# Kernel tuning notes

Hardware: AMD Instinct MI355X
Metric: run time of the kernel (lower is better)

Reference implementation:

```python
import jax, jax.numpy as jnp
import numpy as np

V = 50257   # vocab_size
BLOCK = 1024
D = 768     # n_embd
H = 12      # n_head
L = 2       # n_layer
B = 4
T = 1024
EPS = 1e-5


def _ln(x, g, b):
    mu = jnp.mean(x, axis=-1, keepdims=True)
    var = jnp.var(x, axis=-1, keepdims=True)
    return (x - mu) * jax.lax.rsqrt(var + EPS) * g + b


def setup_inputs() -> dict:
    key = jax.random.key(0)
    ks = jax.random.split(key, 10)
    def n(k, shape, std=0.02):
        return jax.random.normal(k, shape, jnp.float32) * std
    proj_std = (2 * L) ** -0.5  # set_scale init in the torch code
    return dict(
        idx=jax.random.randint(ks[0], (B, T), 0, V),
        layer_num=0,
        wte=n(ks[1], (V, D)),
        wpe=n(ks[2], (BLOCK, D)),
        ln1_g=jnp.ones((L, D)), ln1_b=jnp.zeros((L, D)),
        attn_w=n(ks[3], (L, D, 3 * D)), attn_b=jnp.zeros((L, 3 * D)),
        proj_w=n(ks[4], (L, D, D), proj_std), proj_b=jnp.zeros((L, D)),
        ln2_g=jnp.ones((L, D)), ln2_b=jnp.zeros((L, D)),
        fc_w=n(ks[5], (L, D, 4 * D)), fc_b=jnp.zeros((L, 4 * D)),
        fc2_w=n(ks[6], (L, 4 * D, D), proj_std), fc2_b=jnp.zeros((L, D)),
        lnf_g=jnp.ones((D,)), lnf_b=jnp.zeros((D,)),
        lm_w=n(ks[7], (D, V)),
    )


def _gpt(idx, wte, wpe, ln1_g, ln1_b, attn_w, attn_b, proj_w, proj_b,
         ln2_g, ln2_b, fc_w, fc_b, fc2_w, fc2_b, lnf_g, lnf_b, lm_w):
    b, t = idx.shape
    hd = D // H
    x = wte[idx] + wpe[:t]                      # [B,T,D]
    causal = jnp.tril(jnp.ones((t, t), bool))   # [T,T]
    for l in range(L):
        h = _ln(x, ln1_g[l], ln1_b[l])
        qkv = h @ attn_w[l] + attn_b[l]          # [B,T,3D]
        q, k, v = jnp.split(qkv, 3, axis=-1)
        q = q.reshape(b, t, H, hd)
        k = k.reshape(b, t, H, hd)
        v = v.reshape(b, t, H, hd)
        att = jnp.einsum('bqhd,bkhd->bhqk', q, k) * (1.0 / np.sqrt(hd))
        att = jnp.where(causal, att, -jnp.inf)
        att = jax.nn.softmax(att, axis=-1)
        y = jnp.einsum('bhqk,bkhd->bqhd', att, v).reshape(b, t, D)
        x = x + (y @ proj_w[l] + proj_b[l])
        h2 = _ln(x, ln2_g[l], ln2_b[l])
        h2 = jax.nn.gelu(h2 @ fc_w[l] + fc_b[l], approximate=True)  # tanh GELU
        x = x + (h2 @ fc2_w[l] + fc2_b[l])
    x = _ln(x, lnf_g, lnf_b)
    return x @ lm_w                             # [B,T,V] logits


def reference(idx, layer_num, wte, wpe, ln1_g, ln1_b, attn_w, attn_b,
              proj_w, proj_b, ln2_g, ln2_b, fc_w, fc_b, fc2_w, fc2_b,
              lnf_g, lnf_b, lm_w):
    # layer_num is unused in the forward math (pipeline-stage bookkeeping)
    return _gpt(idx, wte, wpe, ln1_g, ln1_b, attn_w, attn_b, proj_w, proj_b,
                ln2_g, ln2_b, fc_w, fc_b, fc2_w, fc2_b, lnf_g, lnf_b, lm_w)
```

## Files before the change

### kernel.cpp

```cpp
#include <hip/hip_runtime.h>
#include <hip/hip_bf16.h>
#include <cstdint>
#include <cstddef>

typedef __bf16 bf16_t;
typedef __bf16 bf16x8 __attribute__((ext_vector_type(8)));
typedef float f32x4 __attribute__((ext_vector_type(4)));

#define GLB_AS(p) ((__attribute__((address_space(1))) void*)(void*)(p))
#define LDS_AS(p) ((__attribute__((address_space(3))) void*)(p))

__device__ __forceinline__ float wave_red_sum(float v) {
#pragma unroll
  for (int o = 1; o < 64; o <<= 1) v += __shfl_xor(v, o, 64);
  return v;
}

__device__ __forceinline__ float gelu_tanh(float v) {
  float c = 0.7978845608028654f * (v + 0.044715f * v * v * v);
  return 0.5f * v * (1.0f + tanhf(c));
}

__global__ __launch_bounds__(256) void embed_k(const int* __restrict__ idx,
                                               const float* __restrict__ wte,
                                               const float* __restrict__ wpe,
                                               float* __restrict__ x) {
  const int m = blockIdx.x;
  const int tid = threadIdx.x;
  const int tok = idx[m];
  const int t = m & 1023;
#pragma unroll
  for (int i = 0; i < 3; ++i) {
    const int d = tid + i * 256;
    x[(size_t)m * 768 + d] = wte[(size_t)tok * 768 + d] + wpe[(size_t)t * 768 + d];
  }
}

__global__ __launch_bounds__(256) void ln_k(const float* __restrict__ x,
                                            const float* __restrict__ g,
                                            const float* __restrict__ b,
                                            bf16_t* __restrict__ out) {
  const int row = blockIdx.x;
  const int tid = threadIdx.x;
  const float* xr = x + (size_t)row * 768;
  float v0 = xr[tid], v1 = xr[tid + 256], v2 = xr[tid + 512];
  float s = v0 + v1 + v2;
  float q = v0 * v0 + v1 * v1 + v2 * v2;
  s = wave_red_sum(s);
  q = wave_red_sum(q);
  __shared__ float sm[8];
  const int wave = tid >> 6, lane = tid & 63;
  if (lane == 0) { sm[wave] = s; sm[4 + wave] = q; }
  __syncthreads();
  s = sm[0] + sm[1] + sm[2] + sm[3];
  q = sm[4] + sm[5] + sm[6] + sm[7];
  const float mu = s * (1.0f / 768.0f);
  const float var = q * (1.0f / 768.0f) - mu * mu;
  const float rs = rsqrtf(var + 1e-5f);
  bf16_t* orow = out + (size_t)row * 768;
#pragma unroll
  for (int i = 0; i < 3; ++i) {
    const int d = tid + i * 256;
    const float v = (i == 0 ? v0 : (i == 1 ? v1 : v2));
    orow[d] = (bf16_t)((v - mu) * rs * g[d] + b[d]);
  }
}

__global__ __launch_bounds__(256) void transp_k(const float* __restrict__ W,
                                                bf16_t* __restrict__ WT,
                                                int K, int N, int Npad) {
  __shared__ float tile[32][33];
  const int n0 = blockIdx.x * 32, k0 = blockIdx.y * 32;
  const int tx = threadIdx.x, ty = threadIdx.y;
#pragma unroll
  for (int i = 0; i < 4; ++i) {
    const int k = k0 + ty + i * 8, n = n0 + tx;
    tile[ty + i * 8][tx] = (k < K && n < N) ? W[(size_t)k * N + n] : 0.0f;
  }
  __syncthreads();
#pragma unroll
  for (int i = 0; i < 4; ++i) {
    const int n = n0 + ty + i * 8, k = k0 + tx;
    if (n < Npad && k < K) WT[(size_t)n * K + k] = (bf16_t)tile[tx][ty + i * 8];
  }
}

__global__ __launch_bounds__(256) void vtr_k(const bf16_t* __restrict__ qkv,
                                             bf16_t* __restrict__ vt) {
  __shared__ bf16_t tile[64][72];
  const int bh = blockIdx.y;
  const int h = bh % 12, b = bh / 12;
  const int t0 = blockIdx.x * 64;
  const int tx = threadIdx.x & 63;
  const int wv = threadIdx.x >> 6;
#pragma unroll
  for (int i = 0; i < 16; ++i) {
    const int r = wv * 16 + i;
    tile[r][tx] = qkv[(size_t)(b * 1024 + t0 + r) * 2304 + 1536 + h * 64 + tx];
  }
  __syncthreads();
#pragma unroll
  for (int i = 0; i < 16; ++i) {
    const int d = wv * 16 + i;
    vt[((size_t)bh * 64 + d) * 1024 + t0 + tx] = tile[tx][d];
  }
}

template <int EPI>
__global__ __launch_bounds__(256) void gemm_bt(const bf16_t* __restrict__ A,
                                               const bf16_t* __restrict__ BT,
                                               const float* __restrict__ bias,
                                               void* __restrict__ outp,
                                               float* __restrict__ resid,
                                               int M, int N, int K, int Nout) {
  __shared__ __align__(16) bf16_t As[128 * 32];
  __shared__ __align__(16) bf16_t Bs[128 * 32];
  const int tid = threadIdx.x;
  const int lane = tid & 63, wave = tid >> 6;

  const int nmblk = M >> 7;
  const int nwg = gridDim.x;
  const int flat = blockIdx.x;
  const int xcd = flat & 7, rest = flat >> 3;
  const int q8 = nwg >> 3, r8 = nwg & 7;
  const int wgid = (xcd < r8 ? xcd * (q8 + 1) : r8 * (q8 + 1) + (xcd - r8) * q8) + rest;
  const int m0 = (wgid % nmblk) * 128;
  const int n0 = (wgid / nmblk) * 128;

  const int wr = wave >> 1, wc = wave & 1;
  const int fr = lane & 15, fq = lane >> 4;
  const int se = tid * 8;
  const int srow = se >> 5, scol = se & 31;
  const int wvbase = wave * 512;
  f32x4 acc[4][4] = {};

  for (int k0 = 0; k0 < K; k0 += 32) {
#pragma unroll
    for (int r = 0; r < 2; ++r) {
      __builtin_amdgcn_global_load_lds(
          GLB_AS(&A[(size_t)(m0 + srow + r * 64) * K + k0 + scol]),
          LDS_AS(&As[wvbase + r * 2048]), 16, 0, 0);
      __builtin_amdgcn_global_load_lds(
          GLB_AS(&BT[(size_t)(n0 + srow + r * 64) * K + k0 + scol]),
          LDS_AS(&Bs[wvbase + r * 2048]), 16, 0, 0);
    }
    __syncthreads();
    bf16x8 a[4], b[4];
#pragma unroll
    for (int i = 0; i < 4; ++i) {
      a[i] = *(const bf16x8*)(&As[(wr * 64 + i * 16 + fr) * 32 + fq * 8]);
      b[i] = *(const bf16x8*)(&Bs[(wc * 64 + i * 16 + fr) * 32 + fq * 8]);
    }
#pragma unroll
    for (int i = 0; i < 4; ++i)
#pragma unroll
      for (int j = 0; j < 4; ++j)
        acc[i][j] = __builtin_amdgcn_mfma_f32_16x16x32_bf16(a[i], b[j], acc[i][j], 0, 0, 0);
    __syncthreads();
  }

#pragma unroll
  for (int i = 0; i < 4; ++i) {
#pragma unroll
    for (int j = 0; j < 4; ++j) {
      const int r0 = m0 + wr * 64 + i * 16 + fq * 4;
      const int c = n0 + wc * 64 + j * 16 + fr;
      float bv = 0.0f;
      if constexpr (EPI != 3) bv = bias[c];
#pragma unroll
      for (int e = 0; e < 4; ++e) {
        const int r = r0 + e;
        float v = acc[i][j][e] + bv;
        if constexpr (EPI == 0) {
          ((bf16_t*)outp)[(size_t)r * N + c] = (bf16_t)v;
        } else if constexpr (EPI == 1) {
          ((bf16_t*)outp)[(size_t)r * N + c] = (bf16_t)gelu_tanh(v);
        } else if constexpr (EPI == 2) {
          resid[(size_t)r * N + c] += v;
        } else {
          if (c < Nout) ((float*)outp)[(size_t)r * Nout + c] = v;
        }
      }
    }
  }
}

__global__ __launch_bounds__(256) void fattn_k(const bf16_t* __restrict__ qkv,
                                               const bf16_t* __restrict__ vt,
                                               bf16_t* __restrict__ y) {
  __shared__ bf16_t Pl[4][16][40];
  const int wave = threadIdx.x >> 6, lane = threadIdx.x & 63;
  const int wid = blockIdx.x * 4 + wave;
  const int qt = wid & 63;
  const int bh = wid >> 6;
  const int h = bh % 12, b = bh / 12;
  const int fr = lane & 15, fq = lane >> 4;

  const bf16_t* qrow = qkv + (size_t)(b * 1024 + qt * 16 + fr) * 2304 + h * 64;
  const bf16x8 qf0 = *(const bf16x8*)(qrow + fq * 8);
  const bf16x8 qf1 = *(const bf16x8*)(qrow + 32 + fq * 8);

  const bf16_t* kbase = qkv + (size_t)b * 1024 * 2304 + 768 + h * 64 + fq * 8;
  const bf16_t* vbase = vt + ((size_t)bh * 64 + fr) * 1024 + fq * 8;

  f32x4 o[4] = {};
  float mrun[4], lrun[4];
#pragma unroll
  for (int e = 0; e < 4; ++e) { mrun[e] = -1e30f; lrun[e] = 0.0f; }

  const int qg = qt * 16 + fq * 4;
  const int kv_end = qt * 16 + 16;

  for (int kv0 = 0; kv0 < kv_end; kv0 += 32) {
    f32x4 s0 = {}, s1 = {};
    {
      const bf16_t* k0p = kbase + (size_t)(kv0 + fr) * 2304;
      const bf16_t* k1p = kbase + (size_t)(kv0 + 16 + fr) * 2304;
      const bf16x8 kf00 = *(const bf16x8*)(k0p);
      const bf16x8 kf01 = *(const bf16x8*)(k0p + 32);
      const bf16x8 kf10 = *(const bf16x8*)(k1p);
      const bf16x8 kf11 = *(const bf16x8*)(k1p + 32);
      s0 = __builtin_amdgcn_mfma_f32_16x16x32_bf16(qf0, kf00, s0, 0, 0, 0);
      s0 = __builtin_amdgcn_mfma_f32_16x16x32_bf16(qf1, kf01, s0, 0, 0, 0);
      s1 = __builtin_amdgcn_mfma_f32_16x16x32_bf16(qf0, kf10, s1, 0, 0, 0);
      s1 = __builtin_amdgcn_mfma_f32_16x16x32_bf16(qf1, kf11, s1, 0, 0, 0);
    }
    float v0[4], v1[4];
#pragma unroll
    for (int e = 0; e < 4; ++e) {
      v0[e] = (kv0 + fr <= qg + e) ? s0[e] * 0.125f : -1e30f;
      v1[e] = (kv0 + 16 + fr <= qg + e) ? s1[e] * 0.125f : -1e30f;
    }
    float p0[4], p1[4];
#pragma unroll
    for (int e = 0; e < 4; ++e) {
      float mx = fmaxf(v0[e], v1[e]);
      mx = fmaxf(mx, __shfl_xor(mx, 1, 64));
      mx = fmaxf(mx, __shfl_xor(mx, 2, 64));
      mx = fmaxf(mx, __shfl_xor(mx, 4, 64));
      mx = fmaxf(mx, __shfl_xor(mx, 8, 64));
      const float mnew = fmaxf(mrun[e], mx);
      p0[e] = __expf(v0[e] - mnew);
      p1[e] = __expf(v1[e] - mnew);
      float rs = p0[e] + p1[e];
      rs += __shfl_xor(rs, 1, 64);
      rs += __shfl_xor(rs, 2, 64);
      rs += __shfl_xor(rs, 4, 64);
      rs += __shfl_xor(rs, 8, 64);
      const float alpha = __expf(mrun[e] - mnew);
      lrun[e] = lrun[e] * alpha + rs;
      mrun[e] = mnew;
#pragma unroll
      for (int db = 0; db < 4; ++db) o[db][e] *= alpha;
    }
#pragma unroll
    for (int e = 0; e < 4; ++e) {
      Pl[wave][fq * 4 + e][fr] = (bf16_t)p0[e];
      Pl[wave][fq * 4 + e][16 + fr] = (bf16_t)p1[e];
    }
    asm volatile("s_waitcnt lgkmcnt(0)" ::: "memory");
    const bf16x8 pf = *(const bf16x8*)(&Pl[wave][fr][fq * 8]);
#pragma unroll
    for (int db = 0; db < 4; ++db) {
      const bf16x8 vf = *(const bf16x8*)(vbase + (size_t)db * 16 * 1024 + kv0);
      o[db] = __builtin_amdgcn_mfma_f32_16x16x32_bf16(pf, vf, o[db], 0, 0, 0);
    }
  }

#pragma unroll
  for (int db = 0; db < 4; ++db) {
#pragma unroll
    for (int e = 0; e < 4; ++e) {
      const int q = qt * 16 + fq * 4 + e;
      const int d = db * 16 + fr;
      y[(size_t)(b * 1024 + q) * 768 + h * 64 + d] = (bf16_t)(o[db][e] / lrun[e]);
    }
  }
}

extern "C" void kernel_launch(void* const* d_in, const int* in_sizes, int n_in,
                              void* d_out, int out_size, void* d_ws, size_t ws_size,
                              hipStream_t stream) {
  constexpr int Bb = 4, T = 1024, Lg = 2, Vr = 50257, Vp = 50304;
  constexpr int M = Bb * T;

  const int* idx = (const int*)d_in[0];
  const float* wte = (const float*)d_in[2];
  const float* wpe = (const float*)d_in[3];
  const float* ln1_g = (const float*)d_in[4];
  const float* ln1_b = (const float*)d_in[5];
  const float* attn_w = (const float*)d_in[6];
  const float* attn_b = (const float*)d_in[7];
  const float* proj_w = (const float*)d_in[8];
  const float* proj_b = (const float*)d_in[9];
  const float* ln2_g = (const float*)d_in[10];
  const float* ln2_b = (const float*)d_in[11];
  const float* fc_w = (const float*)d_in[12];
  const float* fc_b = (const float*)d_in[13];
  const float* fc2_w = (const float*)d_in[14];
  const float* fc2_b = (const float*)d_in[15];
  const float* lnf_g = (const float*)d_in[16];
  const float* lnf_b = (const float*)d_in[17];
  const float* lm_w = (const float*)d_in[18];
  float* out = (float*)d_out;

  char* wp = (char*)d_ws;
  auto take = [&](size_t n) { char* p = wp; wp += (n + 255) & ~(size_t)255; return p; };
  bf16_t* WqkvT = (bf16_t*)take((size_t)Lg * 2304 * 768 * 2);
  bf16_t* WprojT = (bf16_t*)take((size_t)Lg * 768 * 768 * 2);
  bf16_t* WfcT = (bf16_t*)take((size_t)Lg * 3072 * 768 * 2);
  bf16_t* Wfc2T = (bf16_t*)take((size_t)Lg * 768 * 3072 * 2);
  bf16_t* WlmT = (bf16_t*)take((size_t)Vp * 768 * 2);
  float* xb = (float*)take((size_t)M * 768 * 4);
  bf16_t* hb = (bf16_t*)take((size_t)M * 768 * 2);
  bf16_t* qkvb = (bf16_t*)take((size_t)M * 2304 * 2);
  bf16_t* yb = (bf16_t*)take((size_t)M * 768 * 2);
  bf16_t* actb = (bf16_t*)take((size_t)M * 3072 * 2);
  bf16_t* vtb = (bf16_t*)take((size_t)M * 768 * 2);

  const dim3 tb(32, 8);
  for (int l = 0; l < Lg; ++l) {
    transp_k<<<dim3(2304 / 32, 768 / 32), tb, 0, stream>>>(
        attn_w + (size_t)l * 768 * 2304, WqkvT + (size_t)l * 2304 * 768, 768, 2304, 2304);
    transp_k<<<dim3(768 / 32, 768 / 32), tb, 0, stream>>>(
        proj_w + (size_t)l * 768 * 768, WprojT + (size_t)l * 768 * 768, 768, 768, 768);
    transp_k<<<dim3(3072 / 32, 768 / 32), tb, 0, stream>>>(
        fc_w + (size_t)l * 768 * 3072, WfcT + (size_t)l * 3072 * 768, 768, 3072, 3072);
    transp_k<<<dim3(768 / 32, 3072 / 32), tb, 0, stream>>>(
        fc2_w + (size_t)l * 3072 * 768, Wfc2T + (size_t)l * 768 * 3072, 3072, 768, 768);
  }
  transp_k<<<dim3(Vp / 32, 768 / 32), tb, 0, stream>>>(lm_w, WlmT, 768, Vr, Vp);

  embed_k<<<M, 256, 0, stream>>>(idx, wte, wpe, xb);

  for (int l = 0; l < Lg; ++l) {
    ln_k<<<M, 256, 0, stream>>>(xb, ln1_g + l * 768, ln1_b + l * 768, hb);
    gemm_bt<0><<<(M / 128) * (2304 / 128), 256, 0, stream>>>(
        hb, WqkvT + (size_t)l * 2304 * 768, attn_b + l * 2304, qkvb, nullptr,
        M, 2304, 768, 2304);
    vtr_k<<<dim3(T / 64, Bb * 12), 256, 0, stream>>>(qkvb, vtb);
    fattn_k<<<(Bb * 12 * 64) / 4, 256, 0, stream>>>(qkvb, vtb, yb);
    gemm_bt<2><<<(M / 128) * (768 / 128), 256, 0, stream>>>(
        yb, WprojT + (size_t)l * 768 * 768, proj_b + l * 768, nullptr, xb,
        M, 768, 768, 768);
    ln_k<<<M, 256, 0, stream>>>(xb, ln2_g + l * 768, ln2_b + l * 768, hb);
    gemm_bt<1><<<(M / 128) * (3072 / 128), 256, 0, stream>>>(
        hb, WfcT + (size_t)l * 3072 * 768, fc_b + l * 3072, actb, nullptr,
        M, 3072, 768, 3072);
    gemm_bt<2><<<(M / 128) * (768 / 128), 256, 0, stream>>>(
        actb, Wfc2T + (size_t)l * 768 * 3072, fc2_b + l * 768, nullptr, xb,
        M, 768, 3072, 768);
  }
  ln_k<<<M, 256, 0, stream>>>(xb, lnf_g, lnf_b, hb);
  gemm_bt<3><<<(M / 128) * (Vp / 128), 256, 0, stream>>>(
      hb, WlmT, nullptr, out, nullptr, M, Vp, 768, Vr);
}
```

Baseline: 1.355 ms.

## Add 256x256-tile pipelined GEMM for QKV, FC and LM-head projections

Introduces a new 512-thread GEMM kernel with 256x256 output tiles, BK=64, double-buffered LDS staging via direct global-to-LDS loads, an XOR swizzle to avoid bank conflicts, and interleaved barriers with s_setprio around MFMA phases. The QKV, FC and LM-head GEMMs use it, while the residual-add GEMMs keep the old 128x128 kernel, which is now specialised to the residual epilogue. The vocab padding grows to a multiple of 256 to match the new tile. Larger tiles raise data reuse and overlap loads with compute, at the cost of 128KB LDS per block and fewer blocks for the smaller GEMMs.

```diff
diff --git a/kernel.cpp b/kernel.cpp
--- a/kernel.cpp
+++ b/kernel.cpp
@@ -9,6 +9,7 @@
 
 #define GLB_AS(p) ((__attribute__((address_space(1))) void*)(void*)(p))
 #define LDS_AS(p) ((__attribute__((address_space(3))) void*)(p))
+#define PIN(x) asm volatile("" : "+v"(x))
 
 __device__ __forceinline__ float wave_red_sum(float v) {
 #pragma unroll
@@ -19,6 +20,11 @@
 __device__ __forceinline__ float gelu_tanh(float v) {
   float c = 0.7978845608028654f * (v + 0.044715f * v * v * v);
   return 0.5f * v * (1.0f + tanhf(c));
+}
+
+__device__ __forceinline__ f32x4 mfma16(f32x4 a, f32x4 b, f32x4 c) {
+  return __builtin_amdgcn_mfma_f32_16x16x32_bf16(
+      __builtin_bit_cast(bf16x8, a), __builtin_bit_cast(bf16x8, b), c, 0, 0, 0);
 }
 
 __global__ __launch_bounds__(256) void embed_k(const int* __restrict__ idx,
@@ -107,6 +113,165 @@
 }
 
 template <int EPI>
+__global__ __launch_bounds__(512, 2) void gemm256(const bf16_t* __restrict__ A,
+                                                  const bf16_t* __restrict__ BT,
+                                                  const float* __restrict__ bias,
+                                                  void* __restrict__ outp,
+                                                  int M, int N, int K, int Nout) {
+  __shared__ __align__(16) char lds[131072];
+  const int tid = threadIdx.x;
+  const int lane = tid & 63, wave = tid >> 6;
+  const int wr = wave >> 2, wc = wave & 3;
+  const int fr = lane & 15, fq = lane >> 4;
+
+  const int nmblk = M >> 8;
+  const int nwg = gridDim.x;
+  const int flat = blockIdx.x;
+  const int xcd = flat & 7, rest = flat >> 3;
+  const int q8 = nwg >> 3, r8 = nwg & 7;
+  const int wgid = (xcd < r8 ? xcd * (q8 + 1) : r8 * (q8 + 1) + (xcd - r8) * q8) + rest;
+  const int m0 = (wgid % nmblk) << 8;
+  const int n0 = (wgid / nmblk) << 8;
+
+  const int NT = K >> 6;
+
+  int srow[4], scb[4];
+#pragma unroll
+  for (int u = 0; u < 4; ++u) {
+    const int Lb = u * 8192 + tid * 16;
+    const int s = Lb ^ (((Lb >> 9) & 1) << 5);
+    srow[u] = s >> 7;
+    scb[u] = s & 127;
+  }
+  const char* Abase = (const char*)A;
+  const char* Bbase = (const char*)BT;
+
+  auto stageA = [&](int pi, int u, int tau) {
+    const char* src = Abase + ((size_t)(m0 + srow[u]) * K + tau * 64) * 2 + scb[u];
+    __builtin_amdgcn_global_load_lds(GLB_AS(src),
+        LDS_AS(&lds[pi * 32768 + u * 8192 + wave * 1024]), 16, 0, 0);
+  };
+  auto stageB = [&](int pi, int u, int tau) {
+    const char* src = Bbase + ((size_t)(n0 + srow[u]) * K + tau * 64) * 2 + scb[u];
+    __builtin_amdgcn_global_load_lds(GLB_AS(src),
+        LDS_AS(&lds[65536 + pi * 32768 + u * 8192 + wave * 1024]), 16, 0, 0);
+  };
+  auto rdA = [&](int pi, int msub, int i, int kk) -> f32x4 {
+    const int row = wr * 128 + msub * 64 + i * 16 + fr;
+    const int off = (row * 128 + kk * 64 + fq * 16) ^ (((row >> 2) & 1) << 5);
+    return *(const f32x4*)(&lds[pi * 32768 + off]);
+  };
+  auto rdB = [&](int pi, int j, int kk) -> f32x4 {
+    const int row = wc * 64 + j * 16 + fr;
+    const int off = (row * 128 + kk * 64 + fq * 16) ^ (((row >> 2) & 1) << 5);
+    return *(const f32x4*)(&lds[65536 + pi * 32768 + off]);
+  };
+
+  f32x4 acc[8][4] = {};
+  f32x4 a_[4][2], b_[4][2];
+
+  stageA(0, 0, 0); stageA(0, 1, 0); stageA(0, 2, 0); stageA(0, 3, 0);
+  stageB(0, 0, 0); stageB(0, 1, 0); stageB(0, 2, 0); stageB(0, 3, 0);
+  stageA(1, 0, 1); stageA(1, 2, 1); stageB(1, 0, 1); stageB(1, 1, 1);
+  stageA(1, 1, 1); stageA(1, 3, 1);
+  asm volatile("s_waitcnt vmcnt(6)" ::: "memory");
+  __builtin_amdgcn_s_barrier();
+
+  int pi = 0;
+  for (int tau = 0; tau < NT; ++tau) {
+#pragma unroll
+    for (int i = 0; i < 4; ++i) { a_[i][0] = rdA(pi, 0, i, 0); a_[i][1] = rdA(pi, 0, i, 1); }
+#pragma unroll
+    for (int j = 0; j < 4; ++j) { b_[j][0] = rdB(pi, j, 0); b_[j][1] = rdB(pi, j, 1); }
+#pragma unroll
+    for (int i = 0; i < 4; ++i) { PIN(a_[i][0]); PIN(a_[i][1]); }
+#pragma unroll
+    for (int j = 0; j < 4; ++j) { PIN(b_[j][0]); PIN(b_[j][1]); }
+    if (tau + 1 < NT) { stageB(pi ^ 1, 2, tau + 1); stageB(pi ^ 1, 3, tau + 1); }
+    __builtin_amdgcn_s_barrier();
+    __builtin_amdgcn_s_setprio(1);
+#pragma unroll
+    for (int i = 0; i < 4; ++i)
+#pragma unroll
+      for (int j = 0; j < 2; ++j) {
+        acc[i][j] = mfma16(a_[i][0], b_[j][0], acc[i][j]);
+        acc[i][j] = mfma16(a_[i][1], b_[j][1], acc[i][j]);
+      }
+    __builtin_amdgcn_s_setprio(0);
+    __builtin_amdgcn_s_barrier();
+    if (tau + 2 < NT) { stageA(pi, 0, tau + 2); stageA(pi, 2, tau + 2); }
+    __builtin_amdgcn_s_barrier();
+    __builtin_amdgcn_s_setprio(1);
+#pragma unroll
+    for (int i = 0; i < 4; ++i)
+#pragma unroll
+      for (int j = 0; j < 2; ++j) {
+        acc[i][2 + j] = mfma16(a_[i][0], b_[2 + j][0], acc[i][2 + j]);
+        acc[i][2 + j] = mfma16(a_[i][1], b_[2 + j][1], acc[i][2 + j]);
+      }
+    __builtin_amdgcn_s_setprio(0);
+    __builtin_amdgcn_s_barrier();
+#pragma unroll
+    for (int i = 0; i < 4; ++i) { a_[i][0] = rdA(pi, 1, i, 0); a_[i][1] = rdA(pi, 1, i, 1); }
+#pragma unroll
+    for (int i = 0; i < 4; ++i) { PIN(a_[i][0]); PIN(a_[i][1]); }
+    if (tau + 2 < NT) { stageB(pi, 0, tau + 2); stageB(pi, 1, tau + 2); }
+    __builtin_amdgcn_s_barrier();
+    __builtin_amdgcn_s_setprio(1);
+#pragma unroll
+    for (int i = 0; i < 4; ++i)
+#pragma unroll
+      for (int j = 0; j < 2; ++j) {
+        acc[4 + i][j] = mfma16(a_[i][0], b_[j][0], acc[4 + i][j]);
+        acc[4 + i][j] = mfma16(a_[i][1], b_[j][1], acc[4 + i][j]);
+      }
+    __builtin_amdgcn_s_setprio(0);
+    __builtin_amdgcn_s_barrier();
+    if (tau + 2 < NT) {
+      stageA(pi, 1, tau + 2); stageA(pi, 3, tau + 2);
+      asm volatile("s_waitcnt vmcnt(6)" ::: "memory");
+    } else {
+      asm volatile("s_waitcnt vmcnt(0)" ::: "memory");
+    }
+    __builtin_amdgcn_s_barrier();
+    __builtin_amdgcn_s_setprio(1);
+#pragma unroll
+    for (int i = 0; i < 4; ++i)
+#pragma unroll
+      for (int j = 0; j < 2; ++j) {
+        acc[4 + i][2 + j] = mfma16(a_[i][0], b_[2 + j][0], acc[4 + i][2 + j]);
+        acc[4 + i][2 + j] = mfma16(a_[i][1], b_[2 + j][1], acc[4 + i][2 + j]);
+      }
+    __builtin_amdgcn_s_setprio(0);
+    __builtin_amdgcn_s_barrier();
+    pi ^= 1;
+  }
+
+#pragma unroll
+  for (int i8 = 0; i8 < 8; ++i8) {
+#pragma unroll
+    for (int j4 = 0; j4 < 4; ++j4) {
+      const int r0 = m0 + wr * 128 + i8 * 16 + fq * 4;
+      const int c = n0 + wc * 64 + j4 * 16 + fr;
+      float bv = 0.0f;
+      if constexpr (EPI != 3) bv = bias[c];
+#pragma unroll
+      for (int e = 0; e < 4; ++e) {
+        const int r = r0 + e;
+        float v = acc[i8][j4][e] + bv;
+        if constexpr (EPI == 0) {
+          ((bf16_t*)outp)[(size_t)r * N + c] = (bf16_t)v;
+        } else if constexpr (EPI == 1) {
+          ((bf16_t*)outp)[(size_t)r * N + c] = (bf16_t)gelu_tanh(v);
+        } else {
+          if (c < Nout) ((float*)outp)[(size_t)r * Nout + c] = v;
+        }
+      }
+    }
+  }
+}
+
+template <int EPI>
 __global__ __launch_bounds__(256) void gemm_bt(const bf16_t* __restrict__ A,
                                                const bf16_t* __restrict__ BT,
                                                const float* __restrict__ bias,
@@ -165,21 +330,11 @@
     for (int j = 0; j < 4; ++j) {
       const int r0 = m0 + wr * 64 + i * 16 + fq * 4;
       const int c = n0 + wc * 64 + j * 16 + fr;
-      float bv = 0.0f;
-      if constexpr (EPI != 3) bv = bias[c];
+      const float bv = bias[c];
 #pragma unroll
       for (int e = 0; e < 4; ++e) {
         const int r = r0 + e;
-        float v = acc[i][j][e] + bv;
-        if constexpr (EPI == 0) {
-          ((bf16_t*)outp)[(size_t)r * N + c] = (bf16_t)v;
-        } else if constexpr (EPI == 1) {
-          ((bf16_t*)outp)[(size_t)r * N + c] = (bf16_t)gelu_tanh(v);
-        } else if constexpr (EPI == 2) {
-          resid[(size_t)r * N + c] += v;
-        } else {
-          if (c < Nout) ((float*)outp)[(size_t)r * Nout + c] = v;
-        }
+        resid[(size_t)r * N + c] += acc[i][j][e] + bv;
       }
     }
   }
@@ -281,7 +436,7 @@
 extern "C" void kernel_launch(void* const* d_in, const int* in_sizes, int n_in,
                               void* d_out, int out_size, void* d_ws, size_t ws_size,
                               hipStream_t stream) {
-  constexpr int Bb = 4, T = 1024, Lg = 2, Vr = 50257, Vp = 50304;
+  constexpr int Bb = 4, T = 1024, Lg = 2, Vr = 50257, Vp = 50432;
   constexpr int M = Bb * T;
 
   const int* idx = (const int*)d_in[0];
@@ -335,23 +490,21 @@
 
   for (int l = 0; l < Lg; ++l) {
     ln_k<<<M, 256, 0, stream>>>(xb, ln1_g + l * 768, ln1_b + l * 768, hb);
-    gemm_bt<0><<<(M / 128) * (2304 / 128), 256, 0, stream>>>(
-        hb, WqkvT + (size_t)l * 2304 * 768, attn_b + l * 2304, qkvb, nullptr,
-        M, 2304, 768, 2304);
+    gemm256<0><<<(M / 256) * (2304 / 256), 512, 0, stream>>>(
+        hb, WqkvT + (size_t)l * 2304 * 768, attn_b + l * 2304, qkvb, M, 2304, 768, 2304);
     vtr_k<<<dim3(T / 64, Bb * 12), 256, 0, stream>>>(qkvb, vtb);
     fattn_k<<<(Bb * 12 * 64) / 4, 256, 0, stream>>>(qkvb, vtb, yb);
     gemm_bt<2><<<(M / 128) * (768 / 128), 256, 0, stream>>>(
         yb, WprojT + (size_t)l * 768 * 768, proj_b + l * 768, nullptr, xb,
         M, 768, 768, 768);
     ln_k<<<M, 256, 0, stream>>>(xb, ln2_g + l * 768, ln2_b + l * 768, hb);
-    gemm_bt<1><<<(M / 128) * (3072 / 128), 256, 0, stream>>>(
-        hb, WfcT + (size_t)l * 3072 * 768, fc_b + l * 3072, actb, nullptr,
-        M, 3072, 768, 3072);
+    gemm256<1><<<(M / 256) * (3072 / 256), 512, 0, stream>>>(
+        hb, WfcT + (size_t)l * 3072 * 768, fc_b + l * 3072, actb, M, 3072, 768, 3072);
     gemm_bt<2><<<(M / 128) * (768 / 128), 256, 0, stream>>>(
         actb, Wfc2T + (size_t)l * 768 * 3072, fc2_b + l * 768, nullptr, xb,
         M, 768, 3072, 768);
   }
   ln_k<<<M, 256, 0, stream>>>(xb, lnf_g, lnf_b, hb);
-  gemm_bt<3><<<(M / 128) * (Vp / 128), 256, 0, stream>>>(
-      hb, WlmT, nullptr, out, nullptr, M, Vp, 768, Vr);
-}
+  gemm256<3><<<(M / 256) * (Vp / 256), 512, 0, stream>>>(
+      hb, WlmT, nullptr, out, M, Vp, 768, Vr);
+}
```

After: 1.301 ms. 4.0% less time.

## Replace GEMM with 256x128 double-buffered swizzled-LDS kernel using 8 waves

Applied to the files above, without the earlier changes.

Swaps the 128x128 single-buffered GEMM for a 256x128 tile kernel with 512 threads. It double-buffers LDS with global_load_lds prefetch two K-steps ahead, XOR-swizzles the LDS layout to avoid bank conflicts, and splits the MFMA work into two halves with barriers and setprio. The aim is to overlap global loads with MFMA compute and raise the compute-to-load ratio. Vocab padding grows to a multiple of 128 per the new tiling, and logits use nontemporal stores. Hand-placed waitcnt and barrier scheduling risks correctness and pipeline hazards.

```diff
diff --git a/kernel.cpp b/kernel.cpp
--- a/kernel.cpp
+++ b/kernel.cpp
@@ -9,6 +9,7 @@
 
 #define GLB_AS(p) ((__attribute__((address_space(1))) void*)(void*)(p))
 #define LDS_AS(p) ((__attribute__((address_space(3))) void*)(p))
+#define PIN(x) asm volatile("" : "+v"(x))
 
 __device__ __forceinline__ float wave_red_sum(float v) {
 #pragma unroll
@@ -20,6 +21,13 @@
   float c = 0.7978845608028654f * (v + 0.044715f * v * v * v);
   return 0.5f * v * (1.0f + tanhf(c));
 }
+
+__device__ __forceinline__ f32x4 mfma16(f32x4 a, f32x4 b, f32x4 c) {
+  return __builtin_amdgcn_mfma_f32_16x16x32_bf16(
+      __builtin_bit_cast(bf16x8, a), __builtin_bit_cast(bf16x8, b), c, 0, 0, 0);
+}
+
+__device__ __forceinline__ int swz(int off) { return off ^ ((off >> 3) & 0x30); }
 
 __global__ __launch_bounds__(256) void embed_k(const int* __restrict__ idx,
                                                const float* __restrict__ wte,
@@ -107,66 +115,122 @@
 }
 
 template <int EPI>
-__global__ __launch_bounds__(256) void gemm_bt(const bf16_t* __restrict__ A,
-                                               const bf16_t* __restrict__ BT,
-                                               const float* __restrict__ bias,
-                                               void* __restrict__ outp,
-                                               float* __restrict__ resid,
-                                               int M, int N, int K, int Nout) {
-  __shared__ __align__(16) bf16_t As[128 * 32];
-  __shared__ __align__(16) bf16_t Bs[128 * 32];
+__global__ __launch_bounds__(512, 4) void gemm256(const bf16_t* __restrict__ A,
+                                                  const bf16_t* __restrict__ BT,
+                                                  const float* __restrict__ bias,
+                                                  void* __restrict__ outp,
+                                                  float* __restrict__ resid,
+                                                  int M, int N, int K, int Nout) {
+  __shared__ __align__(16) char lds[49152];
   const int tid = threadIdx.x;
   const int lane = tid & 63, wave = tid >> 6;
-
-  const int nmblk = M >> 7;
+  const int wr = wave >> 2, wc = wave & 3;
+  const int fr = lane & 15, fq = lane >> 4;
+
+  const int nmblk = M >> 8;
   const int nwg = gridDim.x;
   const int flat = blockIdx.x;
   const int xcd = flat & 7, rest = flat >> 3;
   const int q8 = nwg >> 3, r8 = nwg & 7;
   const int wgid = (xcd < r8 ? xcd * (q8 + 1) : r8 * (q8 + 1) + (xcd - r8) * q8) + rest;
-  const int m0 = (wgid % nmblk) * 128;
-  const int n0 = (wgid / nmblk) * 128;
-
-  const int wr = wave >> 1, wc = wave & 1;
-  const int fr = lane & 15, fq = lane >> 4;
-  const int se = tid * 8;
-  const int srow = se >> 5, scol = se & 31;
-  const int wvbase = wave * 512;
-  f32x4 acc[4][4] = {};
-
-  for (int k0 = 0; k0 < K; k0 += 32) {
-#pragma unroll
-    for (int r = 0; r < 2; ++r) {
-      __builtin_amdgcn_global_load_lds(
-          GLB_AS(&A[(size_t)(m0 + srow + r * 64) * K + k0 + scol]),
-          LDS_AS(&As[wvbase + r * 2048]), 16, 0, 0);
-      __builtin_amdgcn_global_load_lds(
-          GLB_AS(&BT[(size_t)(n0 + srow + r * 64) * K + k0 + scol]),
-          LDS_AS(&Bs[wvbase + r * 2048]), 16, 0, 0);
-    }
-    __syncthreads();
-    bf16x8 a[4], b[4];
+  const int m0 = (wgid % nmblk) << 8;
+  const int n0 = (wgid / nmblk) << 7;
+
+  const int NT = K >> 5;
+
+  int srowA[2], scbA[2], srowB, scbB;
+#pragma unroll
+  for (int u = 0; u < 2; ++u) {
+    const int s = swz(u * 8192 + tid * 16);
+    srowA[u] = s >> 6;
+    scbA[u] = s & 63;
+  }
+  {
+    const int s = swz(tid * 16);
+    srowB = s >> 6;
+    scbB = s & 63;
+  }
+  const char* Abase = (const char*)A;
+  const char* Bbase = (const char*)BT;
+
+  int offA[8], offB[2];
+#pragma unroll
+  for (int i = 0; i < 8; ++i) {
+    const int row = wr * 128 + i * 16 + fr;
+    offA[i] = swz(row * 64 + fq * 16);
+  }
+#pragma unroll
+  for (int j = 0; j < 2; ++j) {
+    const int row = wc * 32 + j * 16 + fr;
+    offB[j] = 32768 + swz(row * 64 + fq * 16);
+  }
+
+  auto stageA = [&](int pi, int u, int tau) {
+    const char* src = Abase + ((size_t)(m0 + srowA[u]) * K + tau * 32) * 2 + scbA[u];
+    __builtin_amdgcn_global_load_lds(GLB_AS(src),
+        LDS_AS(&lds[pi * 16384 + u * 8192 + wave * 1024]), 16, 0, 0);
+  };
+  auto stageB = [&](int pi, int tau) {
+    const char* src = Bbase + ((size_t)(n0 + srowB) * K + tau * 32) * 2 + scbB;
+    __builtin_amdgcn_global_load_lds(GLB_AS(src),
+        LDS_AS(&lds[32768 + pi * 8192 + wave * 1024]), 16, 0, 0);
+  };
+
+  f32x4 acc[8][2] = {};
+
+  stageA(0, 0, 0); stageA(0, 1, 0); stageB(0, 0);
+  stageA(1, 0, 1); stageA(1, 1, 1); stageB(1, 1);
+  asm volatile("s_waitcnt vmcnt(3)" ::: "memory");
+  __builtin_amdgcn_s_barrier();
+
+  int pi = 0;
+  for (int tau = 0; tau < NT; ++tau) {
+    const int aoff = pi * 16384, boff = pi * 8192;
+    f32x4 aM[8], bb[2];
+#pragma unroll
+    for (int i = 0; i < 8; ++i) aM[i] = *(const f32x4*)(&lds[offA[i] + aoff]);
+#pragma unroll
+    for (int j = 0; j < 2; ++j) bb[j] = *(const f32x4*)(&lds[offB[j] + boff]);
+#pragma unroll
+    for (int i = 0; i < 8; ++i) PIN(aM[i]);
+    PIN(bb[0]); PIN(bb[1]);
+    __builtin_amdgcn_s_barrier();
+    asm volatile("s_waitcnt lgkmcnt(0)" ::: "memory");
+    __builtin_amdgcn_sched_barrier(0);
+    __builtin_amdgcn_s_setprio(1);
 #pragma unroll
     for (int i = 0; i < 4; ++i) {
-      a[i] = *(const bf16x8*)(&As[(wr * 64 + i * 16 + fr) * 32 + fq * 8]);
-      b[i] = *(const bf16x8*)(&Bs[(wc * 64 + i * 16 + fr) * 32 + fq * 8]);
-    }
-#pragma unroll
-    for (int i = 0; i < 4; ++i)
-#pragma unroll
-      for (int j = 0; j < 4; ++j)
-        acc[i][j] = __builtin_amdgcn_mfma_f32_16x16x32_bf16(a[i], b[j], acc[i][j], 0, 0, 0);
-    __syncthreads();
-  }
-
-#pragma unroll
-  for (int i = 0; i < 4; ++i) {
-#pragma unroll
-    for (int j = 0; j < 4; ++j) {
-      const int r0 = m0 + wr * 64 + i * 16 + fq * 4;
-      const int c = n0 + wc * 64 + j * 16 + fr;
+      acc[i][0] = mfma16(aM[i], bb[0], acc[i][0]);
+      acc[i][1] = mfma16(aM[i], bb[1], acc[i][1]);
+    }
+    __builtin_amdgcn_s_setprio(0);
+    __builtin_amdgcn_s_barrier();
+    if (tau + 2 < NT) {
+      stageA(pi, 0, tau + 2); stageA(pi, 1, tau + 2); stageB(pi, tau + 2);
+      asm volatile("s_waitcnt vmcnt(3)" ::: "memory");
+    } else {
+      asm volatile("s_waitcnt vmcnt(0)" ::: "memory");
+    }
+    __builtin_amdgcn_s_barrier();
+    __builtin_amdgcn_s_setprio(1);
+#pragma unroll
+    for (int i = 0; i < 4; ++i) {
+      acc[4 + i][0] = mfma16(aM[4 + i], bb[0], acc[4 + i][0]);
+      acc[4 + i][1] = mfma16(aM[4 + i], bb[1], acc[4 + i][1]);
+    }
+    __builtin_amdgcn_s_setprio(0);
+    __builtin_amdgcn_s_barrier();
+    pi ^= 1;
+  }
+
+#pragma unroll
+  for (int i = 0; i < 8; ++i) {
+#pragma unroll
+    for (int j = 0; j < 2; ++j) {
+      const int r0 = m0 + wr * 128 + i * 16 + fq * 4;
+      const int c = n0 + wc * 32 + j * 16 + fr;
       float bv = 0.0f;
-      if constexpr (EPI != 3) bv = bias[c];
+      if constexpr (EPI == 0 || EPI == 1 || EPI == 2) bv = bias[c];
 #pragma unroll
       for (int e = 0; e < 4; ++e) {
         const int r = r0 + e;
@@ -178,7 +242,8 @@
         } else if constexpr (EPI == 2) {
           resid[(size_t)r * N + c] += v;
         } else {
-          if (c < Nout) ((float*)outp)[(size_t)r * Nout + c] = v;
+          if (c < Nout)
+            __builtin_nontemporal_store(v, &((float*)outp)[(size_t)r * Nout + c]);
         }
       }
     }
@@ -281,7 +346,7 @@
 extern "C" void kernel_launch(void* const* d_in, const int* in_sizes, int n_in,
                               void* d_out, int out_size, void* d_ws, size_t ws_size,
                               hipStream_t stream) {
-  constexpr int Bb = 4, T = 1024, Lg = 2, Vr = 50257, Vp = 50304;
+  constexpr int Bb = 4, T = 1024, Lg = 2, Vr = 50257, Vp = 50432;
   constexpr int M = Bb * T;
 
   const int* idx = (const int*)d_in[0];
@@ -335,23 +400,23 @@
 
   for (int l = 0; l < Lg; ++l) {
     ln_k<<<M, 256, 0, stream>>>(xb, ln1_g + l * 768, ln1_b + l * 768, hb);
-    gemm_bt<0><<<(M / 128) * (2304 / 128), 256, 0, stream>>>(
+    gemm256<0><<<(M / 256) * (2304 / 128), 512, 0, stream>>>(
         hb, WqkvT + (size_t)l * 2304 * 768, attn_b + l * 2304, qkvb, nullptr,
         M, 2304, 768, 2304);
     vtr_k<<<dim3(T / 64, Bb * 12), 256, 0, stream>>>(qkvb, vtb);
     fattn_k<<<(Bb * 12 * 64) / 4, 256, 0, stream>>>(qkvb, vtb, yb);
-    gemm_bt<2><<<(M / 128) * (768 / 128), 256, 0, stream>>>(
+    gemm256<2><<<(M / 256) * (768 / 128), 512, 0, stream>>>(
         yb, WprojT + (size_t)l * 768 * 768, proj_b + l * 768, nullptr, xb,
         M, 768, 768, 768);
     ln_k<<<M, 256, 0, stream>>>(xb, ln2_g + l * 768, ln2_b + l * 768, hb);
-    gemm_bt<1><<<(M / 128) * (3072 / 128), 256, 0, stream>>>(
+    gemm256<1><<<(M / 256) * (3072 / 128), 512, 0, stream>>>(
         hb, WfcT + (size_t)l * 3072 * 768, fc_b + l * 3072, actb, nullptr,
         M, 3072, 768, 3072);
-    gemm_bt<2><<<(M / 128) * (768 / 128), 256, 0, stream>>>(
+    gemm256<2><<<(M / 256) * (768 / 128), 512, 0, stream>>>(
         actb, Wfc2T + (size_t)l * 768 * 3072, fc2_b + l * 768, nullptr, xb,
         M, 768, 3072, 768);
   }
   ln_k<<<M, 256, 0, stream>>>(xb, lnf_g, lnf_b, hb);
-  gemm_bt<3><<<(M / 128) * (Vp / 128), 256, 0, stream>>>(
+  gemm256<3><<<(M / 256) * (Vp / 128), 512, 0, stream>>>(
       hb, WlmT, nullptr, out, nullptr, M, Vp, 768, Vr);
 }
```

Result: slower. 1.540 ms (+13.7%).

## Add 128x256 double-buffered GEMM with direct-to-LDS loads for wide projections

Applied to the files above, without the earlier changes.

Adds a new 512-thread GEMM kernel with 128x256 tiles. It stages A and B straight into swizzled LDS through global_load_lds, double-buffers the K loop, and splits the MFMA work around the prefetch using s_setprio and explicit waitcnt. The QKV, FC and LM-head GEMMs move to this kernel, and the vocab padding grows to a multiple of 256. The aim is to hide global-load latency, avoid LDS bank conflicts and reuse more data per tile on the large GEMMs. In exchange the kernel uses more LDS and registers, and the LM head does some extra padded work.

```diff
diff --git a/kernel.cpp b/kernel.cpp
--- a/kernel.cpp
+++ b/kernel.cpp
@@ -9,6 +9,7 @@
 
 #define GLB_AS(p) ((__attribute__((address_space(1))) void*)(void*)(p))
 #define LDS_AS(p) ((__attribute__((address_space(3))) void*)(p))
+#define PIN(x) asm volatile("" : "+v"(x))
 
 __device__ __forceinline__ float wave_red_sum(float v) {
 #pragma unroll
@@ -20,6 +21,13 @@
   float c = 0.7978845608028654f * (v + 0.044715f * v * v * v);
   return 0.5f * v * (1.0f + tanhf(c));
 }
+
+__device__ __forceinline__ f32x4 mfma16(f32x4 a, f32x4 b, f32x4 c) {
+  return __builtin_amdgcn_mfma_f32_16x16x32_bf16(
+      __builtin_bit_cast(bf16x8, a), __builtin_bit_cast(bf16x8, b), c, 0, 0, 0);
+}
+
+__device__ __forceinline__ int swz(int off) { return off ^ ((off >> 3) & 0x30); }
 
 __global__ __launch_bounds__(256) void embed_k(const int* __restrict__ idx,
                                                const float* __restrict__ wte,
@@ -107,6 +115,125 @@
 }
 
 template <int EPI>
+__global__ __launch_bounds__(512, 4) void gemm256(const bf16_t* __restrict__ A,
+                                                  const bf16_t* __restrict__ BT,
+                                                  const float* __restrict__ bias,
+                                                  void* __restrict__ outp,
+                                                  int M, int N, int K, int Nout) {
+  __shared__ __align__(16) char lds[49152];
+  const int tid = threadIdx.x;
+  const int lane = tid & 63, wave = tid >> 6;
+  const int wr = wave >> 2, wc = wave & 3;
+  const int fr = lane & 15, fq = lane >> 4;
+
+  const int nmblk = M >> 7;
+  const int nwg = gridDim.x;
+  const int flat = blockIdx.x;
+  const int xcd = flat & 7, rest = flat >> 3;
+  const int q8 = nwg >> 3, r8 = nwg & 7;
+  const int wgid = (xcd < r8 ? xcd * (q8 + 1) : r8 * (q8 + 1) + (xcd - r8) * q8) + rest;
+  const int m0 = (wgid % nmblk) << 7;
+  const int n0 = (wgid / nmblk) << 8;
+
+  const int NT = K >> 5;
+
+  int srow[2], scb[2];
+#pragma unroll
+  for (int u = 0; u < 2; ++u) {
+    const int s = swz(u * 8192 + tid * 16);
+    srow[u] = s >> 6;
+    scb[u] = s & 63;
+  }
+  const char* Abase = (const char*)A;
+  const char* Bbase = (const char*)BT;
+
+  auto stageA = [&](int pi, int tau) {
+    const char* src = Abase + ((size_t)(m0 + srow[0]) * K + tau * 32) * 2 + scb[0];
+    __builtin_amdgcn_global_load_lds(GLB_AS(src),
+        LDS_AS(&lds[pi * 8192 + wave * 1024]), 16, 0, 0);
+  };
+  auto stageB = [&](int pi, int u, int tau) {
+    const char* src = Bbase + ((size_t)(n0 + srow[u]) * K + tau * 32) * 2 + scb[u];
+    __builtin_amdgcn_global_load_lds(GLB_AS(src),
+        LDS_AS(&lds[16384 + pi * 16384 + u * 8192 + wave * 1024]), 16, 0, 0);
+  };
+  auto rdA = [&](int pi, int i) -> f32x4 {
+    const int off = swz((wr * 64 + i * 16 + fr) * 64 + fq * 16);
+    return *(const f32x4*)(&lds[pi * 8192 + off]);
+  };
+  auto rdB = [&](int pi, int j) -> f32x4 {
+    const int off = swz((wc * 64 + j * 16 + fr) * 64 + fq * 16);
+    return *(const f32x4*)(&lds[16384 + pi * 16384 + off]);
+  };
+
+  f32x4 acc[4][4] = {};
+
+  stageA(0, 0); stageB(0, 0, 0); stageB(0, 1, 0);
+  stageA(1, 1); stageB(1, 0, 1); stageB(1, 1, 1);
+  asm volatile("s_waitcnt vmcnt(3)" ::: "memory");
+  __builtin_amdgcn_s_barrier();
+
+  int pi = 0;
+  for (int tau = 0; tau < NT; ++tau) {
+    f32x4 a_[4], b_[4];
+#pragma unroll
+    for (int i = 0; i < 4; ++i) a_[i] = rdA(pi, i);
+#pragma unroll
+    for (int j = 0; j < 4; ++j) b_[j] = rdB(pi, j);
+#pragma unroll
+    for (int i = 0; i < 4; ++i) { PIN(a_[i]); PIN(b_[i]); }
+    __builtin_amdgcn_s_setprio(1);
+#pragma unroll
+    for (int i = 0; i < 4; ++i) {
+      acc[i][0] = mfma16(a_[i], b_[0], acc[i][0]);
+      acc[i][1] = mfma16(a_[i], b_[1], acc[i][1]);
+    }
+    __builtin_amdgcn_s_setprio(0);
+    __builtin_amdgcn_s_barrier();
+    if (tau + 2 < NT) {
+      stageA(pi, tau + 2); stageB(pi, 0, tau + 2); stageB(pi, 1, tau + 2);
+    }
+    __builtin_amdgcn_s_setprio(1);
+#pragma unroll
+    for (int i = 0; i < 4; ++i) {
+      acc[i][2] = mfma16(a_[i], b_[2], acc[i][2]);
+      acc[i][3] = mfma16(a_[i], b_[3], acc[i][3]);
+    }
+    __builtin_amdgcn_s_setprio(0);
+    if (tau + 2 < NT) {
+      asm volatile("s_waitcnt vmcnt(3)" ::: "memory");
+    } else {
+      asm volatile("s_waitcnt vmcnt(0)" ::: "memory");
+    }
+    __builtin_amdgcn_s_barrier();
+    pi ^= 1;
+  }
+
+#pragma unroll
+  for (int i = 0; i < 4; ++i) {
+#pragma unroll
+    for (int j = 0; j < 4; ++j) {
+      const int r0 = m0 + wr * 64 + i * 16 + fq * 4;
+      const int c = n0 + wc * 64 + j * 16 + fr;
+      float bv = 0.0f;
+      if constexpr (EPI != 3) bv = bias[c];
+#pragma unroll
+      for (int e = 0; e < 4; ++e) {
+        const int r = r0 + e;
+        float v = acc[i][j][e] + bv;
+        if constexpr (EPI == 0) {
+          ((bf16_t*)outp)[(size_t)r * N + c] = (bf16_t)v;
+        } else if constexpr (EPI == 1) {
+          ((bf16_t*)outp)[(size_t)r * N + c] = (bf16_t)gelu_tanh(v);
+        } else {
+          if (c < Nout) ((float*)outp)[(size_t)r * Nout + c] = v;
+        }
+      }
+    }
+  }
+}
+
+template <int EPI>
 __global__ __launch_bounds__(256) void gemm_bt(const bf16_t* __restrict__ A,
                                                const bf16_t* __restrict__ BT,
                                                const float* __restrict__ bias,
@@ -165,21 +292,11 @@
     for (int j = 0; j < 4; ++j) {
       const int r0 = m0 + wr * 64 + i * 16 + fq * 4;
       const int c = n0 + wc * 64 + j * 16 + fr;
-      float bv = 0.0f;
-      if constexpr (EPI != 3) bv = bias[c];
+      const float bv = bias[c];
 #pragma unroll
       for (int e = 0; e < 4; ++e) {
         const int r = r0 + e;
-        float v = acc[i][j][e] + bv;
-        if constexpr (EPI == 0) {
-          ((bf16_t*)outp)[(size_t)r * N + c] = (bf16_t)v;
-        } else if constexpr (EPI == 1) {
-          ((bf16_t*)outp)[(size_t)r * N + c] = (bf16_t)gelu_tanh(v);
-        } else if constexpr (EPI == 2) {
-          resid[(size_t)r * N + c] += v;
-        } else {
-          if (c < Nout) ((float*)outp)[(size_t)r * Nout + c] = v;
-        }
+        resid[(size_t)r * N + c] += acc[i][j][e] + bv;
       }
     }
   }
@@ -281,7 +398,7 @@
 extern "C" void kernel_launch(void* const* d_in, const int* in_sizes, int n_in,
                               void* d_out, int out_size, void* d_ws, size_t ws_size,
                               hipStream_t stream) {
-  constexpr int Bb = 4, T = 1024, Lg = 2, Vr = 50257, Vp = 50304;
+  constexpr int Bb = 4, T = 1024, Lg = 2, Vr = 50257, Vp = 50432;
   constexpr int M = Bb * T;
 
   const int* idx = (const int*)d_in[0];
@@ -335,23 +452,21 @@
 
   for (int l = 0; l < Lg; ++l) {
     ln_k<<<M, 256, 0, stream>>>(xb, ln1_g + l * 768, ln1_b + l * 768, hb);
-    gemm_bt<0><<<(M / 128) * (2304 / 128), 256, 0, stream>>>(
-        hb, WqkvT + (size_t)l * 2304 * 768, attn_b + l * 2304, qkvb, nullptr,
-        M, 2304, 768, 2304);
+    gemm256<0><<<(M / 128) * (2304 / 256), 512, 0, stream>>>(
+        hb, WqkvT + (size_t)l * 2304 * 768, attn_b + l * 2304, qkvb, M, 2304, 768, 2304);
     vtr_k<<<dim3(T / 64, Bb * 12), 256, 0, stream>>>(qkvb, vtb);
     fattn_k<<<(Bb * 12 * 64) / 4, 256, 0, stream>>>(qkvb, vtb, yb);
     gemm_bt<2><<<(M / 128) * (768 / 128), 256, 0, stream>>>(
         yb, WprojT + (size_t)l * 768 * 768, proj_b + l * 768, nullptr, xb,
         M, 768, 768, 768);
     ln_k<<<M, 256, 0, stream>>>(xb, ln2_g + l * 768, ln2_b + l * 768, hb);
-    gemm_bt<1><<<(M / 128) * (3072 / 128), 256, 0, stream>>>(
-        hb, WfcT + (size_t)l * 3072 * 768, fc_b + l * 3072, actb, nullptr,
-        M, 3072, 768, 3072);
+    gemm256<1><<<(M / 128) * (3072 / 256), 512, 0, stream>>>(
+        hb, WfcT + (size_t)l * 3072 * 768, fc_b + l * 3072, actb, M, 3072, 768, 3072);
     gemm_bt<2><<<(M / 128) * (768 / 128), 256, 0, stream>>>(
         actb, Wfc2T + (size_t)l * 768 * 3072, fc2_b + l * 768, nullptr, xb,
         M, 768, 3072, 768);
   }
   ln_k<<<M, 256, 0, stream>>>(xb, lnf_g, lnf_b, hb);
-  gemm_bt<3><<<(M / 128) * (Vp / 128), 256, 0, stream>>>(
-      hb, WlmT, nullptr, out, nullptr, M, Vp, 768, Vr);
-}
+  gemm256<3><<<(M / 128) * (Vp / 256), 512, 0, stream>>>(
+      hb, WlmT, nullptr, out, M, Vp, 768, Vr);
+}
```

Measured after the change: 1.290 ms. 4.8% less time.
